# Kernel tuning notes

Hardware: AMD Instinct MI355X
Metric: run time of the kernel (lower is better)

## Reference

```python
import jax, jax.numpy as jnp
import numpy as np

EPS = 1e-10

def setup_inputs() -> dict:
    key = jax.random.key(0)
    kq, kk, kv = jax.random.split(key, 3)
    B, S, D = 8, 4096, 64
    q = jax.random.normal(kq, (B, S, D), dtype=jnp.float32)
    k = jax.random.normal(kk, (B, S, D), dtype=jnp.float32)
    v = jax.random.normal(kv, (B, S, D), dtype=jnp.float32)
    attention_mask = jnp.zeros((B, S, S), dtype=bool)
    return {"q": q, "k": k, "v": v, "attention_mask": attention_mask}

def reference(q, k, v, attention_mask):
    # L2-normalize q and k along feature dim (norm + eps in denominator, per torch code)
    q = q / (jnp.linalg.norm(q, axis=-1, keepdims=True) + EPS)
    k = k / (jnp.linalg.norm(k, axis=-1, keepdims=True) + EPS)
    # [B, S, S] cosine similarity scores
    scores = jnp.einsum('bqd,bkd->bqk', q, k)
    scores = jnp.where(attention_mask, -jnp.inf, scores)
    soft_attention = jax.nn.softmax(scores, axis=-1)
    # dropout_rate = 0.0 -> identity
    output = jnp.einsum('bqk,bkd->bqd', soft_attention, v)
    return (output, soft_attention)
```

## Files before the change

### kernel.cpp

```cpp
#include <hip/hip_runtime.h>
#include <math.h>

#define BB 8
#define SS 4096
#define DD 64
#define NT (SS / 64)

typedef float  f32x4 __attribute__((ext_vector_type(4)));
typedef short  s16x4 __attribute__((ext_vector_type(4)));
typedef short  s16x8 __attribute__((ext_vector_type(8)));
typedef unsigned char u8x16 __attribute__((ext_vector_type(16)));

__device__ __forceinline__ short f2bf(float f) {
  unsigned u = __builtin_bit_cast(unsigned, f);
  u += 0x7FFFu + ((u >> 16) & 1u);
  return (short)(u >> 16);
}

__global__ __launch_bounds__(256) void k_norm(const float* __restrict__ q,
                                              const float* __restrict__ k,
                                              short* __restrict__ qn,
                                              short* __restrict__ kn) {
  const long BS = (long)BB * SS;
  long row = (long)blockIdx.x * 4 + (threadIdx.x >> 6);
  int lane = threadIdx.x & 63;
  const float* src;
  short* dst;
  if (row < BS) { src = q + row * DD; dst = qn + row * DD; }
  else          { src = k + (row - BS) * DD; dst = kn + (row - BS) * DD; }
  float x = src[lane];
  float ss = x * x;
#pragma unroll
  for (int m = 32; m >= 1; m >>= 1) ss += __shfl_xor(ss, m);
  float inv = 1.0f / (sqrtf(ss) + 1e-10f);
  dst[lane] = f2bf(x * inv);
}

__global__ __launch_bounds__(256) void k_vtrans(const float* __restrict__ v,
                                                short* __restrict__ vt) {
  __shared__ short tile[64][65];
  int b = blockIdx.y;
  int s0 = blockIdx.x * 64;
  const float* V = v + ((long)b * SS + s0) * DD;
  int t = threadIdx.x;
#pragma unroll
  for (int i = 0; i < 16; i++) {
    int flat = t + 256 * i;
    int sl = flat >> 6, d = flat & 63;
    tile[sl][d] = f2bf(V[flat]);
  }
  __syncthreads();
  short* VT = vt + (long)b * DD * SS + s0;
#pragma unroll
  for (int i = 0; i < 16; i++) {
    int flat = t + 256 * i;
    int d = flat >> 6, sl = flat & 63;
    VT[(long)d * SS + sl] = tile[sl][d];
  }
}

__global__ __launch_bounds__(256) void k_maskbits(const unsigned char* __restrict__ m,
                                                  unsigned short* __restrict__ bits) {
  long gid = (long)blockIdx.x * 256 + threadIdx.x;
  u8x16 v = __builtin_nontemporal_load((const u8x16*)(m + gid * 16));
  unsigned r = 0;
#pragma unroll
  for (int i = 0; i < 16; i++) r |= (v[i] ? 1u : 0u) << i;
  __builtin_nontemporal_store((unsigned short)r, bits + gid);
}

__global__ __launch_bounds__(256) void k_rowsum(const short* __restrict__ qn,
                                                const short* __restrict__ kn,
                                                const unsigned short* __restrict__ bits,
                                                float* __restrict__ inv_sum) {
  __shared__ __align__(16) short Kt[2][4096];
  int b = blockIdx.x & 7;
  int q0 = (blockIdx.x >> 3) << 6;
  int wid = threadIdx.x >> 6, lane = threadIdx.x & 63;
  int l15 = lane & 15, g = lane >> 4;
  int qr = q0 + (wid << 4);

  const short* Qr = qn + ((long)(b * SS) + qr + l15) * DD;
  s16x8 qf0 = *(const s16x8*)(Qr + 8 * g);
  s16x8 qf1 = *(const s16x8*)(Qr + 32 + 8 * g);

  const short* Kb = kn + (long)b * SS * DD;
  const unsigned long long* B64 =
      (const unsigned long long*)bits + ((long)(b * SS) + qr + l15) * (SS / 64);

  int sr = lane >> 3, sc = lane & 7;
  int r0 = (wid << 4) + sr, r1 = r0 + 8;
  const short* Ksrc0 = Kb + (long)r0 * DD + sc * 8;
  const short* Ksrc1 = Kb + (long)r1 * DD + sc * 8;
  int kd0 = r0 * DD + ((sc ^ sr) << 3);
  int kd1 = r1 * DD + ((sc ^ sr) << 3);

  s16x8 kst0 = *(const s16x8*)Ksrc0;
  s16x8 kst1 = *(const s16x8*)Ksrc1;
  *(s16x8*)&Kt[0][kd0] = kst0;
  *(s16x8*)&Kt[0][kd1] = kst1;
  __syncthreads();

  float acc = 0.f;
  int cur = 0;
  int swk = (l15 & 7);
  for (int t = 0; t < NT; ++t) {
    if (t + 1 < NT) {
      long koff = (long)(t + 1) * 64 * DD;
      kst0 = *(const s16x8*)(Ksrc0 + koff);
      kst1 = *(const s16x8*)(Ksrc1 + koff);
    }
    unsigned long long w64 = B64[t];
    const short* Kc = &Kt[cur][0];
#pragma unroll
    for (int tt = 0; tt < 4; ++tt) {
      const short* krow = Kc + ((tt << 4) + l15) * DD;
      s16x8 a0 = *(const s16x8*)(krow + ((g ^ swk) << 3));
      s16x8 a1 = *(const s16x8*)(krow + (((4 + g) ^ swk) << 3));
      f32x4 c = {0.f, 0.f, 0.f, 0.f};
      c = __builtin_amdgcn_mfma_f32_16x16x32_bf16(a0, qf0, c, 0, 0, 0);
      c = __builtin_amdgcn_mfma_f32_16x16x32_bf16(a1, qf1, c, 0, 0, 0);
#pragma unroll
      for (int r = 0; r < 4; ++r) {
        unsigned bit = (unsigned)(w64 >> ((tt << 4) + (g << 2) + r)) & 1u;
        acc += bit ? 0.f : __expf(c[r]);
      }
    }
    if (t + 1 < NT) {
      short* Kd = &Kt[cur ^ 1][0];
      *(s16x8*)(Kd + kd0) = kst0;
      *(s16x8*)(Kd + kd1) = kst1;
    }
    __syncthreads();
    cur ^= 1;
  }
  acc += __shfl_xor(acc, 16);
  acc += __shfl_xor(acc, 32);
  if (lane < 16) inv_sum[(long)b * SS + qr + l15] = 1.0f / acc;
}

__global__ __launch_bounds__(256) void k_attn(const short* __restrict__ qn,
                                              const short* __restrict__ kn,
                                              const short* __restrict__ vt,
                                              const unsigned short* __restrict__ bits,
                                              const float* __restrict__ inv_sum,
                                              float* __restrict__ O,
                                              float* __restrict__ P) {
  __shared__ __align__(16) short Kt[2][4096];
  __shared__ __align__(16) short Vt[2][4096];
  int b = blockIdx.x & 7;
  int q0 = (blockIdx.x >> 3) << 6;
  int wid = threadIdx.x >> 6, lane = threadIdx.x & 63;
  int l15 = lane & 15, g = lane >> 4;
  int qr = q0 + (wid << 4);

  const short* Qr = qn + ((long)(b * SS) + qr + l15) * DD;
  s16x8 qf0 = *(const s16x8*)(Qr + 8 * g);
  s16x8 qf1 = *(const s16x8*)(Qr + 32 + 8 * g);

  const short* Kb = kn + (long)b * SS * DD;
  const short* Vb = vt + (long)b * DD * SS;
  const unsigned long long* B64 =
      (const unsigned long long*)bits + ((long)(b * SS) + qr + l15) * (SS / 64);
  float inv = inv_sum[(long)b * SS + qr + l15];
  float linv = __logf(inv);
  float* Prow = P + ((long)(b * SS) + qr + l15) * SS;

  int sr = lane >> 3, sc = lane & 7;
  int r0 = (wid << 4) + sr, r1 = r0 + 8;
  const short* Ksrc0 = Kb + (long)r0 * DD + sc * 8;
  const short* Ksrc1 = Kb + (long)r1 * DD + sc * 8;
  const short* Vsrc0 = Vb + (long)r0 * SS + sc * 8;
  const short* Vsrc1 = Vb + (long)r1 * SS + sc * 8;
  int sd0 = r0 * DD + ((sc ^ sr) << 3);
  int sd1 = r1 * DD + ((sc ^ sr) << 3);

  s16x8 kst0 = *(const s16x8*)Ksrc0;
  s16x8 kst1 = *(const s16x8*)Ksrc1;
  s16x8 vst0 = *(const s16x8*)Vsrc0;
  s16x8 vst1 = *(const s16x8*)Vsrc1;
  *(s16x8*)&Kt[0][sd0] = kst0;
  *(s16x8*)&Kt[0][sd1] = kst1;
  *(s16x8*)&Vt[0][sd0] = vst0;
  *(s16x8*)&Vt[0][sd1] = vst1;
  __syncthreads();

  f32x4 o0 = {0, 0, 0, 0}, o1 = {0, 0, 0, 0}, o2 = {0, 0, 0, 0}, o3 = {0, 0, 0, 0};
  int cur = 0;
  int swk = (l15 & 7);
  for (int t = 0; t < NT; ++t) {
    if (t + 1 < NT) {
      long koff = (long)(t + 1) * 64 * DD;
      kst0 = *(const s16x8*)(Ksrc0 + koff);
      kst1 = *(const s16x8*)(Ksrc1 + koff);
      vst0 = *(const s16x8*)(Vsrc0 + (t + 1) * 64);
      vst1 = *(const s16x8*)(Vsrc1 + (t + 1) * 64);
    }
    unsigned long long w64 = B64[t];
    const short* Kc = &Kt[cur][0];
    const short* Vc = &Vt[cur][0];

    f32x4 p[4];
#pragma unroll
    for (int tt = 0; tt < 4; ++tt) {
      const short* krow = Kc + ((tt << 4) + l15) * DD;
      s16x8 a0 = *(const s16x8*)(krow + ((g ^ swk) << 3));
      s16x8 a1 = *(const s16x8*)(krow + (((4 + g) ^ swk) << 3));
      f32x4 c = {0.f, 0.f, 0.f, 0.f};
      c = __builtin_amdgcn_mfma_f32_16x16x32_bf16(a0, qf0, c, 0, 0, 0);
      c = __builtin_amdgcn_mfma_f32_16x16x32_bf16(a1, qf1, c, 0, 0, 0);
#pragma unroll
      for (int r = 0; r < 4; ++r) {
        unsigned bit = (unsigned)(w64 >> ((tt << 4) + (g << 2) + r)) & 1u;
        p[tt][r] = bit ? 0.f : __expf(c[r] + linv);
      }
      __builtin_nontemporal_store(p[tt],
          (f32x4*)(Prow + (t << 6) + (tt << 4) + (g << 2)));
    }

    s16x8 pa0, pa1;
#pragma unroll
    for (int j = 0; j < 4; ++j) {
      pa0[j] = f2bf(p[0][j]); pa0[4 + j] = f2bf(p[1][j]);
      pa1[j] = f2bf(p[2][j]); pa1[4 + j] = f2bf(p[3][j]);
    }

#pragma unroll
    for (int n = 0; n < 4; ++n) {
      const short* vrow = Vc + ((n << 4) + l15) * DD;
      int g2 = g >> 1, hh = (g & 1) << 2;
      s16x4 lo0 = *(const s16x4*)(vrow + (((g2    ) ^ swk) << 3) + hh);
      s16x4 hi0 = *(const s16x4*)(vrow + (((g2 + 2) ^ swk) << 3) + hh);
      s16x4 lo1 = *(const s16x4*)(vrow + (((g2 + 4) ^ swk) << 3) + hh);
      s16x4 hi1 = *(const s16x4*)(vrow + (((g2 + 6) ^ swk) << 3) + hh);
      s16x8 vf0 = __builtin_shufflevector(lo0, hi0, 0, 1, 2, 3, 4, 5, 6, 7);
      s16x8 vf1 = __builtin_shufflevector(lo1, hi1, 0, 1, 2, 3, 4, 5, 6, 7);
      f32x4* on = (n == 0) ? &o0 : (n == 1) ? &o1 : (n == 2) ? &o2 : &o3;
      *on = __builtin_amdgcn_mfma_f32_16x16x32_bf16(pa0, vf0, *on, 0, 0, 0);
      *on = __builtin_amdgcn_mfma_f32_16x16x32_bf16(pa1, vf1, *on, 0, 0, 0);
    }

    if (t + 1 < NT) {
      short* Kd = &Kt[cur ^ 1][0];
      short* Vd = &Vt[cur ^ 1][0];
      *(s16x8*)(Kd + sd0) = kst0;
      *(s16x8*)(Kd + sd1) = kst1;
      *(s16x8*)(Vd + sd0) = vst0;
      *(s16x8*)(Vd + sd1) = vst1;
    }
    __syncthreads();
    cur ^= 1;
  }

  float* Ob = O + ((long)(b * SS) + qr) * DD;
#pragma unroll
  for (int r = 0; r < 4; ++r) {
    int row = (g << 2) + r;
    Ob[row * DD +  0 + l15] = o0[r];
    Ob[row * DD + 16 + l15] = o1[r];
    Ob[row * DD + 32 + l15] = o2[r];
    Ob[row * DD + 48 + l15] = o3[r];
  }
}

extern "C" void kernel_launch(void* const* d_in, const int* in_sizes, int n_in,
                              void* d_out, int out_size, void* d_ws, size_t ws_size,
                              hipStream_t stream) {
  const float* q = (const float*)d_in[0];
  const float* k = (const float*)d_in[1];
  const float* v = (const float*)d_in[2];
  const unsigned char* mask = (const unsigned char*)d_in[3];

  const long BSD = (long)BB * SS * DD;
  short* qn = (short*)d_ws;
  short* kn = qn + BSD;
  short* vtp = kn + BSD;
  float* inv_sum = (float*)(vtp + BSD);
  unsigned short* bits = (unsigned short*)(inv_sum + (long)BB * SS);

  float* O = (float*)d_out;
  float* P = O + BSD;

  k_norm<<<dim3(2 * BB * SS / 4), dim3(256), 0, stream>>>(q, k, qn, kn);
  k_vtrans<<<dim3(SS / 64, BB), dim3(256), 0, stream>>>(v, vtp);
  k_maskbits<<<dim3((int)((long)BB * SS * SS / 16 / 256)), dim3(256), 0, stream>>>(mask, bits);
  k_rowsum<<<dim3(BB * SS / 64), dim3(256), 0, stream>>>(qn, kn, bits, inv_sum);
  k_attn<<<dim3(BB * SS / 64), dim3(256), 0, stream>>>(qn, kn, vtp, bits, inv_sum, O, P);
}
```

Before: 252.7 us.

## Fuse mask bit-packing, row-sum, and attention passes into one kernel

New measurement: 309.0 us. 22.3% more time.

```diff
diff --git a/kernel.cpp b/kernel.cpp
--- a/kernel.cpp
+++ b/kernel.cpp
@@ -59,21 +59,17 @@
   }
 }
 
-__global__ __launch_bounds__(256) void k_maskbits(const unsigned char* __restrict__ m,
-                                                  unsigned short* __restrict__ bits) {
-  long gid = (long)blockIdx.x * 256 + threadIdx.x;
-  u8x16 v = __builtin_nontemporal_load((const u8x16*)(m + gid * 16));
-  unsigned r = 0;
-#pragma unroll
-  for (int i = 0; i < 16; i++) r |= (v[i] ? 1u : 0u) << i;
-  __builtin_nontemporal_store((unsigned short)r, bits + gid);
-}
-
-__global__ __launch_bounds__(256) void k_rowsum(const short* __restrict__ qn,
-                                                const short* __restrict__ kn,
-                                                const unsigned short* __restrict__ bits,
-                                                float* __restrict__ inv_sum) {
+__global__ __launch_bounds__(256) void k_fused(const short* __restrict__ qn,
+                                               const short* __restrict__ kn,
+                                               const short* __restrict__ vt,
+                                               const unsigned char* __restrict__ mask,
+                                               float* __restrict__ O,
+                                               float* __restrict__ P) {
   __shared__ __align__(16) short Kt[2][4096];
+  __shared__ __align__(16) short Vt[2][4096];
+  __shared__ __align__(16) unsigned long long bitsL[NT * 64];
+  unsigned short* bits16 = (unsigned short*)bitsL;
+
   int b = blockIdx.x & 7;
   int q0 = (blockIdx.x >> 3) << 6;
   int wid = threadIdx.x >> 6, lane = threadIdx.x & 63;
@@ -85,86 +81,7 @@
   s16x8 qf1 = *(const s16x8*)(Qr + 32 + 8 * g);
 
   const short* Kb = kn + (long)b * SS * DD;
-  const unsigned long long* B64 =
-      (const unsigned long long*)bits + ((long)(b * SS) + qr + l15) * (SS / 64);
-
-  int sr = lane >> 3, sc = lane & 7;
-  int r0 = (wid << 4) + sr, r1 = r0 + 8;
-  const short* Ksrc0 = Kb + (long)r0 * DD + sc * 8;
-  const short* Ksrc1 = Kb + (long)r1 * DD + sc * 8;
-  int kd0 = r0 * DD + ((sc ^ sr) << 3);
-  int kd1 = r1 * DD + ((sc ^ sr) << 3);
-
-  s16x8 kst0 = *(const s16x8*)Ksrc0;
-  s16x8 kst1 = *(const s16x8*)Ksrc1;
-  *(s16x8*)&Kt[0][kd0] = kst0;
-  *(s16x8*)&Kt[0][kd1] = kst1;
-  __syncthreads();
-
-  float acc = 0.f;
-  int cur = 0;
-  int swk = (l15 & 7);
-  for (int t = 0; t < NT; ++t) {
-    if (t + 1 < NT) {
-      long koff = (long)(t + 1) * 64 * DD;
-      kst0 = *(const s16x8*)(Ksrc0 + koff);
-      kst1 = *(const s16x8*)(Ksrc1 + koff);
-    }
-    unsigned long long w64 = B64[t];
-    const short* Kc = &Kt[cur][0];
-#pragma unroll
-    for (int tt = 0; tt < 4; ++tt) {
-      const short* krow = Kc + ((tt << 4) + l15) * DD;
-      s16x8 a0 = *(const s16x8*)(krow + ((g ^ swk) << 3));
-      s16x8 a1 = *(const s16x8*)(krow + (((4 + g) ^ swk) << 3));
-      f32x4 c = {0.f, 0.f, 0.f, 0.f};
-      c = __builtin_amdgcn_mfma_f32_16x16x32_bf16(a0, qf0, c, 0, 0, 0);
-      c = __builtin_amdgcn_mfma_f32_16x16x32_bf16(a1, qf1, c, 0, 0, 0);
-#pragma unroll
-      for (int r = 0; r < 4; ++r) {
-        unsigned bit = (unsigned)(w64 >> ((tt << 4) + (g << 2) + r)) & 1u;
-        acc += bit ? 0.f : __expf(c[r]);
-      }
-    }
-    if (t + 1 < NT) {
-      short* Kd = &Kt[cur ^ 1][0];
-      *(s16x8*)(Kd + kd0) = kst0;
-      *(s16x8*)(Kd + kd1) = kst1;
-    }
-    __syncthreads();
-    cur ^= 1;
-  }
-  acc += __shfl_xor(acc, 16);
-  acc += __shfl_xor(acc, 32);
-  if (lane < 16) inv_sum[(long)b * SS + qr + l15] = 1.0f / acc;
-}
-
-__global__ __launch_bounds__(256) void k_attn(const short* __restrict__ qn,
-                                              const short* __restrict__ kn,
-                                              const short* __restrict__ vt,
-                                              const unsigned short* __restrict__ bits,
-                                              const float* __restrict__ inv_sum,
-                                              float* __restrict__ O,
-                                              float* __restrict__ P) {
-  __shared__ __align__(16) short Kt[2][4096];
-  __shared__ __align__(16) short Vt[2][4096];
-  int b = blockIdx.x & 7;
-  int q0 = (blockIdx.x >> 3) << 6;
-  int wid = threadIdx.x >> 6, lane = threadIdx.x & 63;
-  int l15 = lane & 15, g = lane >> 4;
-  int qr = q0 + (wid << 4);
-
-  const short* Qr = qn + ((long)(b * SS) + qr + l15) * DD;
-  s16x8 qf0 = *(const s16x8*)(Qr + 8 * g);
-  s16x8 qf1 = *(const s16x8*)(Qr + 32 + 8 * g);
-
-  const short* Kb = kn + (long)b * SS * DD;
   const short* Vb = vt + (long)b * DD * SS;
-  const unsigned long long* B64 =
-      (const unsigned long long*)bits + ((long)(b * SS) + qr + l15) * (SS / 64);
-  float inv = inv_sum[(long)b * SS + qr + l15];
-  float linv = __logf(inv);
-  float* Prow = P + ((long)(b * SS) + qr + l15) * SS;
 
   int sr = lane >> 3, sc = lane & 7;
   int r0 = (wid << 4) + sr, r1 = r0 + 8;
@@ -174,9 +91,74 @@
   const short* Vsrc1 = Vb + (long)r1 * SS + sc * 8;
   int sd0 = r0 * DD + ((sc ^ sr) << 3);
   int sd1 = r1 * DD + ((sc ^ sr) << 3);
-
+  int swk = l15 & 7;
+
+  int mrow = (wid << 4) + (lane >> 2);
+  int mpiece = lane & 3;
+  const unsigned char* Msrc = mask + ((long)(b * SS) + q0 + mrow) * SS + mpiece * 16;
+
+  u8x16 mCur = __builtin_nontemporal_load((const u8x16*)Msrc);
+  u8x16 mNext = __builtin_nontemporal_load((const u8x16*)(Msrc + 64));
   s16x8 kst0 = *(const s16x8*)Ksrc0;
   s16x8 kst1 = *(const s16x8*)Ksrc1;
+  {
+    unsigned bv = 0;
+#pragma unroll
+    for (int i = 0; i < 16; i++) bv |= (mCur[i] ? 1u : 0u) << i;
+    bits16[(0 * 64 + mrow) * 4 + mpiece] = (unsigned short)bv;
+  }
+  *(s16x8*)&Kt[0][sd0] = kst0;
+  *(s16x8*)&Kt[0][sd1] = kst1;
+  __syncthreads();
+
+  float acc = 0.f;
+  int cur = 0;
+  for (int t = 0; t < NT; ++t) {
+    if (t + 1 < NT) {
+      long koff = (long)(t + 1) * 64 * DD;
+      kst0 = *(const s16x8*)(Ksrc0 + koff);
+      kst1 = *(const s16x8*)(Ksrc1 + koff);
+    }
+    u8x16 mFar = mNext;
+    if (t + 2 < NT)
+      mFar = __builtin_nontemporal_load((const u8x16*)(Msrc + (long)(t + 2) * 64));
+    if (t + 1 < NT) {
+      unsigned bv = 0;
+#pragma unroll
+      for (int i = 0; i < 16; i++) bv |= (mNext[i] ? 1u : 0u) << i;
+      bits16[((t + 1) * 64 + mrow) * 4 + mpiece] = (unsigned short)bv;
+    }
+    unsigned long long w64 = bitsL[t * 64 + (wid << 4) + l15];
+    const short* Kc = &Kt[cur][0];
+#pragma unroll
+    for (int tt = 0; tt < 4; ++tt) {
+      const short* krow = Kc + ((tt << 4) + l15) * DD;
+      s16x8 a0 = *(const s16x8*)(krow + ((g ^ swk) << 3));
+      s16x8 a1 = *(const s16x8*)(krow + (((4 + g) ^ swk) << 3));
+      f32x4 c = {0.f, 0.f, 0.f, 0.f};
+      c = __builtin_amdgcn_mfma_f32_16x16x32_bf16(a0, qf0, c, 0, 0, 0);
+      c = __builtin_amdgcn_mfma_f32_16x16x32_bf16(a1, qf1, c, 0, 0, 0);
+#pragma unroll
+      for (int r = 0; r < 4; ++r) {
+        unsigned bit = (unsigned)(w64 >> ((tt << 4) + (g << 2) + r)) & 1u;
+        acc += bit ? 0.f : __expf(c[r]);
+      }
+    }
+    if (t + 1 < NT) {
+      short* Kd = &Kt[cur ^ 1][0];
+      *(s16x8*)(Kd + sd0) = kst0;
+      *(s16x8*)(Kd + sd1) = kst1;
+    }
+    __syncthreads();
+    cur ^= 1;
+    mNext = mFar;
+  }
+  acc += __shfl_xor(acc, 16);
+  acc += __shfl_xor(acc, 32);
+  float linv = -__logf(acc);
+
+  kst0 = *(const s16x8*)Ksrc0;
+  kst1 = *(const s16x8*)Ksrc1;
   s16x8 vst0 = *(const s16x8*)Vsrc0;
   s16x8 vst1 = *(const s16x8*)Vsrc1;
   *(s16x8*)&Kt[0][sd0] = kst0;
@@ -185,9 +167,9 @@
   *(s16x8*)&Vt[0][sd1] = vst1;
   __syncthreads();
 
+  float* Prow = P + ((long)(b * SS) + qr + l15) * SS;
   f32x4 o0 = {0, 0, 0, 0}, o1 = {0, 0, 0, 0}, o2 = {0, 0, 0, 0}, o3 = {0, 0, 0, 0};
-  int cur = 0;
-  int swk = (l15 & 7);
+  cur = 0;
   for (int t = 0; t < NT; ++t) {
     if (t + 1 < NT) {
       long koff = (long)(t + 1) * 64 * DD;
@@ -196,7 +178,7 @@
       vst0 = *(const s16x8*)(Vsrc0 + (t + 1) * 64);
       vst1 = *(const s16x8*)(Vsrc1 + (t + 1) * 64);
     }
-    unsigned long long w64 = B64[t];
+    unsigned long long w64 = bitsL[t * 64 + (wid << 4) + l15];
     const short* Kc = &Kt[cur][0];
     const short* Vc = &Vt[cur][0];
 
@@ -275,15 +257,11 @@
   short* qn = (short*)d_ws;
   short* kn = qn + BSD;
   short* vtp = kn + BSD;
-  float* inv_sum = (float*)(vtp + BSD);
-  unsigned short* bits = (unsigned short*)(inv_sum + (long)BB * SS);
 
   float* O = (float*)d_out;
   float* P = O + BSD;
 
   k_norm<<<dim3(2 * BB * SS / 4), dim3(256), 0, stream>>>(q, k, qn, kn);
   k_vtrans<<<dim3(SS / 64, BB), dim3(256), 0, stream>>>(v, vtp);
-  k_maskbits<<<dim3((int)((long)BB * SS * SS / 16 / 256)), dim3(256), 0, stream>>>(mask, bits);
-  k_rowsum<<<dim3(BB * SS / 64), dim3(256), 0, stream>>>(qn, kn, bits, inv_sum);
-  k_attn<<<dim3(BB * SS / 64), dim3(256), 0, stream>>>(qn, kn, vtp, bits, inv_sum, O, P);
-}
+  k_fused<<<dim3(BB * SS / 64), dim3(256), 0, stream>>>(qn, kn, vtp, mask, O, P);
+}
```

## Split key dimension in half across blocks with atomic output accumulation

Applied to the files above, without the earlier changes.

After: 262.3 us. 1.04x slower.

```diff
diff --git a/kernel.cpp b/kernel.cpp
--- a/kernel.cpp
+++ b/kernel.cpp
@@ -4,7 +4,8 @@
 #define BB 8
 #define SS 4096
 #define DD 64
-#define NT (SS / 64)
+#define NTH 32
+#define LOG2E 1.4426950408889634f
 
 typedef float  f32x4 __attribute__((ext_vector_type(4)));
 typedef short  s16x4 __attribute__((ext_vector_type(4)));
@@ -26,18 +27,20 @@
   int lane = threadIdx.x & 63;
   const float* src;
   short* dst;
-  if (row < BS) { src = q + row * DD; dst = qn + row * DD; }
-  else          { src = k + (row - BS) * DD; dst = kn + (row - BS) * DD; }
+  float sc;
+  if (row < BS) { src = q + row * DD; dst = qn + row * DD; sc = LOG2E; }
+  else          { src = k + (row - BS) * DD; dst = kn + (row - BS) * DD; sc = 1.0f; }
   float x = src[lane];
   float ss = x * x;
 #pragma unroll
   for (int m = 32; m >= 1; m >>= 1) ss += __shfl_xor(ss, m);
-  float inv = 1.0f / (sqrtf(ss) + 1e-10f);
+  float inv = sc / (sqrtf(ss) + 1e-10f);
   dst[lane] = f2bf(x * inv);
 }
 
 __global__ __launch_bounds__(256) void k_vtrans(const float* __restrict__ v,
-                                                short* __restrict__ vt) {
+                                                short* __restrict__ vt,
+                                                float* __restrict__ O) {
   __shared__ short tile[64][65];
   int b = blockIdx.y;
   int s0 = blockIdx.x * 64;
@@ -49,6 +52,13 @@
     int sl = flat >> 6, d = flat & 63;
     tile[sl][d] = f2bf(V[flat]);
   }
+  {
+    f32x4 z = {0.f, 0.f, 0.f, 0.f};
+    f32x4* O4 = (f32x4*)O;
+    long tid = (long)(blockIdx.y * gridDim.x + blockIdx.x) * 256 + t;
+#pragma unroll
+    for (int j = 0; j < 4; j++) O4[j * 131072 + tid] = z;
+  }
   __syncthreads();
   short* VT = vt + (long)b * DD * SS + s0;
 #pragma unroll
@@ -72,10 +82,12 @@
 __global__ __launch_bounds__(256) void k_rowsum(const short* __restrict__ qn,
                                                 const short* __restrict__ kn,
                                                 const unsigned short* __restrict__ bits,
-                                                float* __restrict__ inv_sum) {
+                                                float* __restrict__ accP) {
   __shared__ __align__(16) short Kt[2][4096];
   int b = blockIdx.x & 7;
-  int q0 = (blockIdx.x >> 3) << 6;
+  int half = (blockIdx.x >> 3) & 1;
+  int q0 = (blockIdx.x >> 4) << 6;
+  int t0 = half * NTH;
   int wid = threadIdx.x >> 6, lane = threadIdx.x & 63;
   int l15 = lane & 15, g = lane >> 4;
   int qr = q0 + (wid << 4);
@@ -84,7 +96,7 @@
   s16x8 qf0 = *(const s16x8*)(Qr + 8 * g);
   s16x8 qf1 = *(const s16x8*)(Qr + 32 + 8 * g);
 
-  const short* Kb = kn + (long)b * SS * DD;
+  const short* Kb = kn + (long)b * SS * DD + (long)t0 * 64 * DD;
   const unsigned long long* B64 =
       (const unsigned long long*)bits + ((long)(b * SS) + qr + l15) * (SS / 64);
 
@@ -94,6 +106,7 @@
   const short* Ksrc1 = Kb + (long)r1 * DD + sc * 8;
   int kd0 = r0 * DD + ((sc ^ sr) << 3);
   int kd1 = r1 * DD + ((sc ^ sr) << 3);
+  int swk = l15 & 7;
 
   s16x8 kst0 = *(const s16x8*)Ksrc0;
   s16x8 kst1 = *(const s16x8*)Ksrc1;
@@ -103,14 +116,13 @@
 
   float acc = 0.f;
   int cur = 0;
-  int swk = (l15 & 7);
-  for (int t = 0; t < NT; ++t) {
-    if (t + 1 < NT) {
+  for (int t = 0; t < NTH; ++t) {
+    if (t + 1 < NTH) {
       long koff = (long)(t + 1) * 64 * DD;
       kst0 = *(const s16x8*)(Ksrc0 + koff);
       kst1 = *(const s16x8*)(Ksrc1 + koff);
     }
-    unsigned long long w64 = B64[t];
+    unsigned long long w64 = B64[t0 + t];
     const short* Kc = &Kt[cur][0];
 #pragma unroll
     for (int tt = 0; tt < 4; ++tt) {
@@ -123,10 +135,10 @@
 #pragma unroll
       for (int r = 0; r < 4; ++r) {
         unsigned bit = (unsigned)(w64 >> ((tt << 4) + (g << 2) + r)) & 1u;
-        acc += bit ? 0.f : __expf(c[r]);
+        acc += bit ? 0.f : exp2f(c[r]);
       }
     }
-    if (t + 1 < NT) {
+    if (t + 1 < NTH) {
       short* Kd = &Kt[cur ^ 1][0];
       *(s16x8*)(Kd + kd0) = kst0;
       *(s16x8*)(Kd + kd1) = kst1;
@@ -136,20 +148,23 @@
   }
   acc += __shfl_xor(acc, 16);
   acc += __shfl_xor(acc, 32);
-  if (lane < 16) inv_sum[(long)b * SS + qr + l15] = 1.0f / acc;
+  if (lane < 16)
+    accP[(long)half * (BB * SS) + (long)b * SS + qr + l15] = acc;
 }
 
 __global__ __launch_bounds__(256) void k_attn(const short* __restrict__ qn,
                                               const short* __restrict__ kn,
                                               const short* __restrict__ vt,
                                               const unsigned short* __restrict__ bits,
-                                              const float* __restrict__ inv_sum,
+                                              const float* __restrict__ accP,
                                               float* __restrict__ O,
                                               float* __restrict__ P) {
   __shared__ __align__(16) short Kt[2][4096];
   __shared__ __align__(16) short Vt[2][4096];
   int b = blockIdx.x & 7;
-  int q0 = (blockIdx.x >> 3) << 6;
+  int half = (blockIdx.x >> 3) & 1;
+  int q0 = (blockIdx.x >> 4) << 6;
+  int t0 = half * NTH;
   int wid = threadIdx.x >> 6, lane = threadIdx.x & 63;
   int l15 = lane & 15, g = lane >> 4;
   int qr = q0 + (wid << 4);
@@ -158,13 +173,13 @@
   s16x8 qf0 = *(const s16x8*)(Qr + 8 * g);
   s16x8 qf1 = *(const s16x8*)(Qr + 32 + 8 * g);
 
-  const short* Kb = kn + (long)b * SS * DD;
-  const short* Vb = vt + (long)b * DD * SS;
+  const short* Kb = kn + (long)b * SS * DD + (long)t0 * 64 * DD;
+  const short* Vb = vt + (long)b * DD * SS + t0 * 64;
   const unsigned long long* B64 =
       (const unsigned long long*)bits + ((long)(b * SS) + qr + l15) * (SS / 64);
-  float inv = inv_sum[(long)b * SS + qr + l15];
-  float linv = __logf(inv);
-  float* Prow = P + ((long)(b * SS) + qr + l15) * SS;
+  long rowid = (long)b * SS + qr + l15;
+  float linv2 = -__log2f(accP[rowid] + accP[(long)(BB * SS) + rowid]);
+  float* Prow = P + rowid * SS;
 
   int sr = lane >> 3, sc = lane & 7;
   int r0 = (wid << 4) + sr, r1 = r0 + 8;
@@ -174,6 +189,7 @@
   const short* Vsrc1 = Vb + (long)r1 * SS + sc * 8;
   int sd0 = r0 * DD + ((sc ^ sr) << 3);
   int sd1 = r1 * DD + ((sc ^ sr) << 3);
+  int swk = l15 & 7;
 
   s16x8 kst0 = *(const s16x8*)Ksrc0;
   s16x8 kst1 = *(const s16x8*)Ksrc1;
@@ -187,16 +203,15 @@
 
   f32x4 o0 = {0, 0, 0, 0}, o1 = {0, 0, 0, 0}, o2 = {0, 0, 0, 0}, o3 = {0, 0, 0, 0};
   int cur = 0;
-  int swk = (l15 & 7);
-  for (int t = 0; t < NT; ++t) {
-    if (t + 1 < NT) {
+  for (int t = 0; t < NTH; ++t) {
+    if (t + 1 < NTH) {
       long koff = (long)(t + 1) * 64 * DD;
       kst0 = *(const s16x8*)(Ksrc0 + koff);
       kst1 = *(const s16x8*)(Ksrc1 + koff);
       vst0 = *(const s16x8*)(Vsrc0 + (t + 1) * 64);
       vst1 = *(const s16x8*)(Vsrc1 + (t + 1) * 64);
     }
-    unsigned long long w64 = B64[t];
+    unsigned long long w64 = B64[t0 + t];
     const short* Kc = &Kt[cur][0];
     const short* Vc = &Vt[cur][0];
 
@@ -212,10 +227,10 @@
 #pragma unroll
       for (int r = 0; r < 4; ++r) {
         unsigned bit = (unsigned)(w64 >> ((tt << 4) + (g << 2) + r)) & 1u;
-        p[tt][r] = bit ? 0.f : __expf(c[r] + linv);
+        p[tt][r] = bit ? 0.f : exp2f(c[r] + linv2);
       }
       __builtin_nontemporal_store(p[tt],
-          (f32x4*)(Prow + (t << 6) + (tt << 4) + (g << 2)));
+          (f32x4*)(Prow + ((t0 + t) << 6) + (tt << 4) + (g << 2)));
     }
 
     s16x8 pa0, pa1;
@@ -240,7 +255,7 @@
       *on = __builtin_amdgcn_mfma_f32_16x16x32_bf16(pa1, vf1, *on, 0, 0, 0);
     }
 
-    if (t + 1 < NT) {
+    if (t + 1 < NTH) {
       short* Kd = &Kt[cur ^ 1][0];
       short* Vd = &Vt[cur ^ 1][0];
       *(s16x8*)(Kd + sd0) = kst0;
@@ -256,10 +271,10 @@
 #pragma unroll
   for (int r = 0; r < 4; ++r) {
     int row = (g << 2) + r;
-    Ob[row * DD +  0 + l15] = o0[r];
-    Ob[row * DD + 16 + l15] = o1[r];
-    Ob[row * DD + 32 + l15] = o2[r];
-    Ob[row * DD + 48 + l15] = o3[r];
+    atomicAdd(&Ob[row * DD +  0 + l15], o0[r]);
+    atomicAdd(&Ob[row * DD + 16 + l15], o1[r]);
+    atomicAdd(&Ob[row * DD + 32 + l15], o2[r]);
+    atomicAdd(&Ob[row * DD + 48 + l15], o3[r]);
   }
 }
 
@@ -275,15 +290,15 @@
   short* qn = (short*)d_ws;
   short* kn = qn + BSD;
   short* vtp = kn + BSD;
-  float* inv_sum = (float*)(vtp + BSD);
-  unsigned short* bits = (unsigned short*)(inv_sum + (long)BB * SS);
+  unsigned short* bits = (unsigned short*)(vtp + BSD);
+  float* accP = (float*)(bits + (long)BB * SS * (SS / 16));
 
   float* O = (float*)d_out;
   float* P = O + BSD;
 
   k_norm<<<dim3(2 * BB * SS / 4), dim3(256), 0, stream>>>(q, k, qn, kn);
-  k_vtrans<<<dim3(SS / 64, BB), dim3(256), 0, stream>>>(v, vtp);
+  k_vtrans<<<dim3(SS / 64, BB), dim3(256), 0, stream>>>(v, vtp, O);
   k_maskbits<<<dim3((int)((long)BB * SS * SS / 16 / 256)), dim3(256), 0, stream>>>(mask, bits);
-  k_rowsum<<<dim3(BB * SS / 64), dim3(256), 0, stream>>>(qn, kn, bits, inv_sum);
-  k_attn<<<dim3(BB * SS / 64), dim3(256), 0, stream>>>(qn, kn, vtp, bits, inv_sum, O, P);
-}
+  k_rowsum<<<dim3(2 * BB * SS / 64), dim3(256), 0, stream>>>(qn, kn, bits, accP);
+  k_attn<<<dim3(2 * BB * SS / 64), dim3(256), 0, stream>>>(qn, kn, vtp, bits, accP, O, P);
+}
```

## Fuse mask bit-packing into rowsum and use exp2 with log2e-prescaled queries

Applied to the files above, without the earlier changes.

Result: slower. 291.8 us (+15.5%).

```diff
diff --git a/kernel.cpp b/kernel.cpp
--- a/kernel.cpp
+++ b/kernel.cpp
@@ -5,6 +5,7 @@
 #define SS 4096
 #define DD 64
 #define NT (SS / 64)
+#define LOG2E 1.4426950408889634f
 
 typedef float  f32x4 __attribute__((ext_vector_type(4)));
 typedef short  s16x4 __attribute__((ext_vector_type(4)));
@@ -15,6 +16,12 @@
   unsigned u = __builtin_bit_cast(unsigned, f);
   u += 0x7FFFu + ((u >> 16) & 1u);
   return (short)(u >> 16);
+}
+
+__device__ __forceinline__ unsigned pk_bf16(float lo, float hi) {
+  unsigned r;
+  asm("v_cvt_pk_bf16_f32 %0, %1, %2" : "=v"(r) : "v"(lo), "v"(hi));
+  return r;
 }
 
 __global__ __launch_bounds__(256) void k_norm(const float* __restrict__ q,
@@ -26,13 +33,14 @@
   int lane = threadIdx.x & 63;
   const float* src;
   short* dst;
-  if (row < BS) { src = q + row * DD; dst = qn + row * DD; }
-  else          { src = k + (row - BS) * DD; dst = kn + (row - BS) * DD; }
+  float sc;
+  if (row < BS) { src = q + row * DD; dst = qn + row * DD; sc = LOG2E; }
+  else          { src = k + (row - BS) * DD; dst = kn + (row - BS) * DD; sc = 1.0f; }
   float x = src[lane];
   float ss = x * x;
 #pragma unroll
   for (int m = 32; m >= 1; m >>= 1) ss += __shfl_xor(ss, m);
-  float inv = 1.0f / (sqrtf(ss) + 1e-10f);
+  float inv = sc / (sqrtf(ss) + 1e-10f);
   dst[lane] = f2bf(x * inv);
 }
 
@@ -59,41 +67,48 @@
   }
 }
 
-__global__ __launch_bounds__(256) void k_maskbits(const unsigned char* __restrict__ m,
-                                                  unsigned short* __restrict__ bits) {
-  long gid = (long)blockIdx.x * 256 + threadIdx.x;
-  u8x16 v = __builtin_nontemporal_load((const u8x16*)(m + gid * 16));
-  unsigned r = 0;
-#pragma unroll
-  for (int i = 0; i < 16; i++) r |= (v[i] ? 1u : 0u) << i;
-  __builtin_nontemporal_store((unsigned short)r, bits + gid);
-}
-
 __global__ __launch_bounds__(256) void k_rowsum(const short* __restrict__ qn,
                                                 const short* __restrict__ kn,
-                                                const unsigned short* __restrict__ bits,
-                                                float* __restrict__ inv_sum) {
+                                                const unsigned char* __restrict__ mask,
+                                                unsigned short* __restrict__ bits16,
+                                                float* __restrict__ accG) {
   __shared__ __align__(16) short Kt[2][4096];
+  __shared__ __align__(16) unsigned long long bitsL[64 * 64];
+  unsigned short* bitsLu16 = (unsigned short*)bitsL;
+
   int b = blockIdx.x & 7;
   int q0 = (blockIdx.x >> 3) << 6;
-  int wid = threadIdx.x >> 6, lane = threadIdx.x & 63;
+  int tid = threadIdx.x;
+  int wid = tid >> 6, lane = tid & 63;
   int l15 = lane & 15, g = lane >> 4;
   int qr = q0 + (wid << 4);
+
+  const unsigned char* Mb = mask + ((long)(b * SS) + q0) * SS;
+  unsigned short* Bg = bits16 + ((long)(b * SS) + q0) * 256 + tid;
+#pragma unroll 4
+  for (int i = 0; i < 64; ++i) {
+    u8x16 m = __builtin_nontemporal_load((const u8x16*)(Mb + (long)i * SS + tid * 16));
+    unsigned r = 0;
+#pragma unroll
+    for (int j = 0; j < 16; ++j) r |= (m[j] ? 1u : 0u) << j;
+    int cs = ((tid >> 2) ^ i) & 63;
+    bitsLu16[i * 256 + cs * 4 + (tid & 3)] = (unsigned short)r;
+    __builtin_nontemporal_store((unsigned short)r, Bg + i * 256);
+  }
 
   const short* Qr = qn + ((long)(b * SS) + qr + l15) * DD;
   s16x8 qf0 = *(const s16x8*)(Qr + 8 * g);
   s16x8 qf1 = *(const s16x8*)(Qr + 32 + 8 * g);
 
   const short* Kb = kn + (long)b * SS * DD;
-  const unsigned long long* B64 =
-      (const unsigned long long*)bits + ((long)(b * SS) + qr + l15) * (SS / 64);
-
   int sr = lane >> 3, sc = lane & 7;
   int r0 = (wid << 4) + sr, r1 = r0 + 8;
   const short* Ksrc0 = Kb + (long)r0 * DD + sc * 8;
   const short* Ksrc1 = Kb + (long)r1 * DD + sc * 8;
   int kd0 = r0 * DD + ((sc ^ sr) << 3);
   int kd1 = r1 * DD + ((sc ^ sr) << 3);
+  int swk = l15 & 7;
+  int brow = (wid << 4) + l15;
 
   s16x8 kst0 = *(const s16x8*)Ksrc0;
   s16x8 kst1 = *(const s16x8*)Ksrc1;
@@ -103,27 +118,40 @@
 
   float acc = 0.f;
   int cur = 0;
-  int swk = (l15 & 7);
   for (int t = 0; t < NT; ++t) {
     if (t + 1 < NT) {
       long koff = (long)(t + 1) * 64 * DD;
       kst0 = *(const s16x8*)(Ksrc0 + koff);
       kst1 = *(const s16x8*)(Ksrc1 + koff);
     }
-    unsigned long long w64 = B64[t];
+    unsigned long long w64 = bitsL[brow * 64 + ((t ^ brow) & 63)];
     const short* Kc = &Kt[cur][0];
-#pragma unroll
-    for (int tt = 0; tt < 4; ++tt) {
-      const short* krow = Kc + ((tt << 4) + l15) * DD;
-      s16x8 a0 = *(const s16x8*)(krow + ((g ^ swk) << 3));
-      s16x8 a1 = *(const s16x8*)(krow + (((4 + g) ^ swk) << 3));
-      f32x4 c = {0.f, 0.f, 0.f, 0.f};
-      c = __builtin_amdgcn_mfma_f32_16x16x32_bf16(a0, qf0, c, 0, 0, 0);
-      c = __builtin_amdgcn_mfma_f32_16x16x32_bf16(a1, qf1, c, 0, 0, 0);
-#pragma unroll
-      for (int r = 0; r < 4; ++r) {
-        unsigned bit = (unsigned)(w64 >> ((tt << 4) + (g << 2) + r)) & 1u;
-        acc += bit ? 0.f : __expf(c[r]);
+    if (__builtin_expect(__all(w64 == 0ull), 1)) {
+#pragma unroll
+      for (int tt = 0; tt < 4; ++tt) {
+        const short* krow = Kc + ((tt << 4) + l15) * DD;
+        s16x8 a0 = *(const s16x8*)(krow + ((g ^ swk) << 3));
+        s16x8 a1 = *(const s16x8*)(krow + (((4 + g) ^ swk) << 3));
+        f32x4 c = {0.f, 0.f, 0.f, 0.f};
+        c = __builtin_amdgcn_mfma_f32_16x16x32_bf16(a0, qf0, c, 0, 0, 0);
+        c = __builtin_amdgcn_mfma_f32_16x16x32_bf16(a1, qf1, c, 0, 0, 0);
+#pragma unroll
+        for (int r = 0; r < 4; ++r) acc += exp2f(c[r]);
+      }
+    } else {
+#pragma unroll
+      for (int tt = 0; tt < 4; ++tt) {
+        const short* krow = Kc + ((tt << 4) + l15) * DD;
+        s16x8 a0 = *(const s16x8*)(krow + ((g ^ swk) << 3));
+        s16x8 a1 = *(const s16x8*)(krow + (((4 + g) ^ swk) << 3));
+        f32x4 c = {0.f, 0.f, 0.f, 0.f};
+        c = __builtin_amdgcn_mfma_f32_16x16x32_bf16(a0, qf0, c, 0, 0, 0);
+        c = __builtin_amdgcn_mfma_f32_16x16x32_bf16(a1, qf1, c, 0, 0, 0);
+#pragma unroll
+        for (int r = 0; r < 4; ++r) {
+          unsigned bit = (unsigned)(w64 >> ((tt << 4) + (g << 2) + r)) & 1u;
+          acc += bit ? 0.f : exp2f(c[r]);
+        }
       }
     }
     if (t + 1 < NT) {
@@ -136,14 +164,14 @@
   }
   acc += __shfl_xor(acc, 16);
   acc += __shfl_xor(acc, 32);
-  if (lane < 16) inv_sum[(long)b * SS + qr + l15] = 1.0f / acc;
+  if (lane < 16) accG[(long)b * SS + qr + l15] = acc;
 }
 
 __global__ __launch_bounds__(256) void k_attn(const short* __restrict__ qn,
                                               const short* __restrict__ kn,
                                               const short* __restrict__ vt,
                                               const unsigned short* __restrict__ bits,
-                                              const float* __restrict__ inv_sum,
+                                              const float* __restrict__ accG,
                                               float* __restrict__ O,
                                               float* __restrict__ P) {
   __shared__ __align__(16) short Kt[2][4096];
@@ -160,11 +188,10 @@
 
   const short* Kb = kn + (long)b * SS * DD;
   const short* Vb = vt + (long)b * DD * SS;
-  const unsigned long long* B64 =
-      (const unsigned long long*)bits + ((long)(b * SS) + qr + l15) * (SS / 64);
-  float inv = inv_sum[(long)b * SS + qr + l15];
-  float linv = __logf(inv);
-  float* Prow = P + ((long)(b * SS) + qr + l15) * SS;
+  long rowid = (long)b * SS + qr + l15;
+  const unsigned long long* B64 = (const unsigned long long*)bits + rowid * (SS / 64);
+  float linv2 = -__log2f(accG[rowid]);
+  float* Prow = P + rowid * SS;
 
   int sr = lane >> 3, sc = lane & 7;
   int r0 = (wid << 4) + sr, r1 = r0 + 8;
@@ -174,6 +201,7 @@
   const short* Vsrc1 = Vb + (long)r1 * SS + sc * 8;
   int sd0 = r0 * DD + ((sc ^ sr) << 3);
   int sd1 = r1 * DD + ((sc ^ sr) << 3);
+  int swk = l15 & 7;
 
   s16x8 kst0 = *(const s16x8*)Ksrc0;
   s16x8 kst1 = *(const s16x8*)Ksrc1;
@@ -187,7 +215,6 @@
 
   f32x4 o0 = {0, 0, 0, 0}, o1 = {0, 0, 0, 0}, o2 = {0, 0, 0, 0}, o3 = {0, 0, 0, 0};
   int cur = 0;
-  int swk = (l15 & 7);
   for (int t = 0; t < NT; ++t) {
     if (t + 1 < NT) {
       long koff = (long)(t + 1) * 64 * DD;
@@ -201,29 +228,48 @@
     const short* Vc = &Vt[cur][0];
 
     f32x4 p[4];
-#pragma unroll
-    for (int tt = 0; tt < 4; ++tt) {
-      const short* krow = Kc + ((tt << 4) + l15) * DD;
-      s16x8 a0 = *(const s16x8*)(krow + ((g ^ swk) << 3));
-      s16x8 a1 = *(const s16x8*)(krow + (((4 + g) ^ swk) << 3));
-      f32x4 c = {0.f, 0.f, 0.f, 0.f};
-      c = __builtin_amdgcn_mfma_f32_16x16x32_bf16(a0, qf0, c, 0, 0, 0);
-      c = __builtin_amdgcn_mfma_f32_16x16x32_bf16(a1, qf1, c, 0, 0, 0);
-#pragma unroll
-      for (int r = 0; r < 4; ++r) {
-        unsigned bit = (unsigned)(w64 >> ((tt << 4) + (g << 2) + r)) & 1u;
-        p[tt][r] = bit ? 0.f : __expf(c[r] + linv);
+    if (__builtin_expect(__all(w64 == 0ull), 1)) {
+#pragma unroll
+      for (int tt = 0; tt < 4; ++tt) {
+        const short* krow = Kc + ((tt << 4) + l15) * DD;
+        s16x8 a0 = *(const s16x8*)(krow + ((g ^ swk) << 3));
+        s16x8 a1 = *(const s16x8*)(krow + (((4 + g) ^ swk) << 3));
+        f32x4 c = {0.f, 0.f, 0.f, 0.f};
+        c = __builtin_amdgcn_mfma_f32_16x16x32_bf16(a0, qf0, c, 0, 0, 0);
+        c = __builtin_amdgcn_mfma_f32_16x16x32_bf16(a1, qf1, c, 0, 0, 0);
+#pragma unroll
+        for (int r = 0; r < 4; ++r) p[tt][r] = exp2f(c[r] + linv2);
+        __builtin_nontemporal_store(p[tt],
+            (f32x4*)(Prow + (t << 6) + (tt << 4) + (g << 2)));
       }
-      __builtin_nontemporal_store(p[tt],
-          (f32x4*)(Prow + (t << 6) + (tt << 4) + (g << 2)));
-    }
-
-    s16x8 pa0, pa1;
-#pragma unroll
-    for (int j = 0; j < 4; ++j) {
-      pa0[j] = f2bf(p[0][j]); pa0[4 + j] = f2bf(p[1][j]);
-      pa1[j] = f2bf(p[2][j]); pa1[4 + j] = f2bf(p[3][j]);
-    }
+    } else {
+#pragma unroll
+      for (int tt = 0; tt < 4; ++tt) {
+        const short* krow = Kc + ((tt << 4) + l15) * DD;
+        s16x8 a0 = *(const s16x8*)(krow + ((g ^ swk) << 3));
+        s16x8 a1 = *(const s16x8*)(krow + (((4 + g) ^ swk) << 3));
+        f32x4 c = {0.f, 0.f, 0.f, 0.f};
+        c = __builtin_amdgcn_mfma_f32_16x16x32_bf16(a0, qf0, c, 0, 0, 0);
+        c = __builtin_amdgcn_mfma_f32_16x16x32_bf16(a1, qf1, c, 0, 0, 0);
+#pragma unroll
+        for (int r = 0; r < 4; ++r) {
+          unsigned bit = (unsigned)(w64 >> ((tt << 4) + (g << 2) + r)) & 1u;
+          p[tt][r] = bit ? 0.f : exp2f(c[r] + linv2);
+        }
+        __builtin_nontemporal_store(p[tt],
+            (f32x4*)(Prow + (t << 6) + (tt << 4) + (g << 2)));
+      }
+    }
+
+    union { s16x8 v; unsigned u[4]; } pa0, pa1;
+    pa0.u[0] = pk_bf16(p[0][0], p[0][1]);
+    pa0.u[1] = pk_bf16(p[0][2], p[0][3]);
+    pa0.u[2] = pk_bf16(p[1][0], p[1][1]);
+    pa0.u[3] = pk_bf16(p[1][2], p[1][3]);
+    pa1.u[0] = pk_bf16(p[2][0], p[2][1]);
+    pa1.u[1] = pk_bf16(p[2][2], p[2][3]);
+    pa1.u[2] = pk_bf16(p[3][0], p[3][1]);
+    pa1.u[3] = pk_bf16(p[3][2], p[3][3]);
 
 #pragma unroll
     for (int n = 0; n < 4; ++n) {
@@ -236,8 +282,8 @@
       s16x8 vf0 = __builtin_shufflevector(lo0, hi0, 0, 1, 2, 3, 4, 5, 6, 7);
       s16x8 vf1 = __builtin_shufflevector(lo1, hi1, 0, 1, 2, 3, 4, 5, 6, 7);
       f32x4* on = (n == 0) ? &o0 : (n == 1) ? &o1 : (n == 2) ? &o2 : &o3;
-      *on = __builtin_amdgcn_mfma_f32_16x16x32_bf16(pa0, vf0, *on, 0, 0, 0);
-      *on = __builtin_amdgcn_mfma_f32_16x16x32_bf16(pa1, vf1, *on, 0, 0, 0);
+      *on = __builtin_amdgcn_mfma_f32_16x16x32_bf16(pa0.v, vf0, *on, 0, 0, 0);
+      *on = __builtin_amdgcn_mfma_f32_16x16x32_bf16(pa1.v, vf1, *on, 0, 0, 0);
     }
 
     if (t + 1 < NT) {
@@ -275,15 +321,14 @@
   short* qn = (short*)d_ws;
   short* kn = qn + BSD;
   short* vtp = kn + BSD;
-  float* inv_sum = (float*)(vtp + BSD);
-  unsigned short* bits = (unsigned short*)(inv_sum + (long)BB * SS);
+  unsigned short* bits = (unsigned short*)(vtp + BSD);
+  float* accG = (float*)(bits + (long)BB * SS * 256);
 
   float* O = (float*)d_out;
   float* P = O + BSD;
 
   k_norm<<<dim3(2 * BB * SS / 4), dim3(256), 0, stream>>>(q, k, qn, kn);
   k_vtrans<<<dim3(SS / 64, BB), dim3(256), 0, stream>>>(v, vtp);
-  k_maskbits<<<dim3((int)((long)BB * SS * SS / 16 / 256)), dim3(256), 0, stream>>>(mask, bits);
-  k_rowsum<<<dim3(BB * SS / 64), dim3(256), 0, stream>>>(qn, kn, bits, inv_sum);
-  k_attn<<<dim3(BB * SS / 64), dim3(256), 0, stream>>>(qn, kn, vtp, bits, inv_sum, O, P);
-}
+  k_rowsum<<<dim3(BB * SS / 64), dim3(256), 0, stream>>>(qn, kn, mask, bits, accG);
+  k_attn<<<dim3(BB * SS / 64), dim3(256), 0, stream>>>(qn, kn, vtp, bits, accG, O, P);
+}
```
